# Kernel tuning notes

Hardware: AMD Instinct MI355X
Metric: run time of the kernel (lower is better)

Reference implementation:

```python
import jax, jax.numpy as jnp
import numpy as np

D_MODEL = 1024
N_HEADS = 16
D_K = D_MODEL // N_HEADS

def setup_inputs() -> dict:
    key = jax.random.key(0)
    ks = jax.random.split(key, 9)
    s = 1.0 / np.sqrt(D_MODEL)
    inp = {"x": jax.random.normal(ks[0], (2, 2048, D_MODEL), dtype=jnp.float32)}
    for i, name in enumerate(["q", "k", "v", "o"]):
        inp[f"W{name}"] = jax.random.uniform(ks[1 + i], (D_MODEL, D_MODEL), dtype=jnp.float32, minval=-s, maxval=s)
        inp[f"b{name}"] = jax.random.uniform(ks[5 + i], (D_MODEL,), dtype=jnp.float32, minval=-s, maxval=s)
    return inp

def _split_heads(t):
    B, S, _ = t.shape
    return t.reshape(B, S, N_HEADS, D_K).transpose(0, 2, 1, 3)  # [B,H,S,d_k]

def reference(x, Wq, bq, Wk, bk, Wv, bv, Wo, bo):
    # QKV projections (torch Linear: x @ W.T + b)
    q = _split_heads(x @ Wq.T + bq)
    k = _split_heads(x @ Wk.T + bk)
    v = _split_heads(x @ Wv.T + bv)
    scores = jnp.einsum('bhqd,bhkd->bhqk', q, k) / jnp.sqrt(jnp.asarray(D_K, x.dtype))
    probs = jax.nn.softmax(scores, axis=-1)
    attn = jnp.einsum('bhqk,bhkd->bhqd', probs, v)  # [B,H,S,d_k]
    B, H, S, _ = attn.shape
    merged = attn.transpose(0, 2, 1, 3).reshape(B, S, D_MODEL)
    return merged @ Wo.T + bo
```

## Files before the change

kernel.cpp:

```cpp
#include <hip/hip_runtime.h>
#include <hip/hip_bf16.h>
#include <stdint.h>


#define LOG2E 1.4426950408889634f

typedef float f32x4 __attribute__((ext_vector_type(4)));
typedef float f32x16 __attribute__((ext_vector_type(16)));
typedef short bf16x8 __attribute__((ext_vector_type(8)));
typedef short bf16x4 __attribute__((ext_vector_type(4)));
typedef unsigned int u32x2 __attribute__((ext_vector_type(2)));

__device__ __forceinline__ unsigned short f2bf(float f) {
  __hip_bfloat16 h = __float2bfloat16(f);
  return reinterpret_cast<unsigned short&>(h);
}

#define GLDS(g, l) __builtin_amdgcn_global_load_lds(                          \
    (const __attribute__((address_space(1))) void*)(g),                       \
    (__attribute__((address_space(3))) void*)(l), 16, 0, 0)

__global__ __launch_bounds__(256) void k_conv(const float* __restrict__ src,
                                              unsigned short* __restrict__ dst,
                                              int n4, float scale) {
  int i = blockIdx.x * 256 + threadIdx.x;
  const int stride = gridDim.x * 256;
  for (; i < n4; i += stride) {
    float4 v = ((const float4*)src)[i];
    ushort4 o;
    o.x = f2bf(v.x * scale);
    o.y = f2bf(v.y * scale);
    o.z = f2bf(v.z * scale);
    o.w = f2bf(v.w * scale);
    ((ushort4*)dst)[i] = o;
  }
}

__global__ __launch_bounds__(256) void k_convW(const float* __restrict__ wq,
                                               const float* __restrict__ wk,
                                               const float* __restrict__ wv,
                                               const float* __restrict__ wo,
                                               unsigned short* __restrict__ dq,
                                               unsigned short* __restrict__ dk,
                                               unsigned short* __restrict__ dv,
                                               unsigned short* __restrict__ dw) {
  const int m = blockIdx.y;
  const float* src = (m == 0) ? wq : (m == 1) ? wk : (m == 2) ? wv : wo;
  unsigned short* dst = (m == 0) ? dq : (m == 1) ? dk : (m == 2) ? dv : dw;
  const float scale = (m == 0) ? (0.125f * LOG2E) : 1.0f;
  int i = blockIdx.x * 256 + threadIdx.x;
  float4 v = ((const float4*)src)[i];
  ushort4 o;
  o.x = f2bf(v.x * scale);
  o.y = f2bf(v.y * scale);
  o.z = f2bf(v.z * scale);
  o.w = f2bf(v.w * scale);
  ((ushort4*)dst)[i] = o;
}

__global__ __launch_bounds__(256) void k_bias(const float* __restrict__ bq,
                                              const float* __restrict__ bk,
                                              const float* __restrict__ bv,
                                              float* __restrict__ out) {
  int i = blockIdx.x * 256 + threadIdx.x;
  float v;
  if (i < 1024) v = bq[i] * (0.125f * LOG2E);
  else if (i < 2048) v = bk[i - 1024];
  else v = bv[i - 2048];
  out[i] = v;
}

template <int MODE>
__global__ __launch_bounds__(256) void k_gemm(const unsigned short* __restrict__ A,
                                              const unsigned short* __restrict__ B,
                                              const float* __restrict__ bias,
                                              void* __restrict__ outp) {
  __shared__ unsigned short As[128 * 32];
  __shared__ unsigned short Bs[128 * 32];
  const int tid = threadIdx.x;
  const int lane = tid & 63, wid = tid >> 6;
  const int wr = wid >> 1, wc = wid & 1;
  const int r = lane & 15, g = lane >> 4;
  const int bm = blockIdx.x, bn = blockIdx.y;

  const unsigned short* gA = A + (size_t)bm * 128 * 1024;
  const unsigned short* gB = B + (size_t)bn * 128 * 1024;
  const int row0 = tid >> 2, cg = (tid & 3) * 8;

  f32x4 acc[4][4] = {};

  for (int k0 = 0; k0 < 1024; k0 += 32) {
    __syncthreads();
    GLDS(gA + (size_t)row0 * 1024 + k0 + cg,        As + row0 * 32 + cg);
    GLDS(gA + (size_t)(row0 + 64) * 1024 + k0 + cg, As + (row0 + 64) * 32 + cg);
    GLDS(gB + (size_t)row0 * 1024 + k0 + cg,        Bs + row0 * 32 + cg);
    GLDS(gB + (size_t)(row0 + 64) * 1024 + k0 + cg, Bs + (row0 + 64) * 32 + cg);
    __syncthreads();

    bf16x8 af[4], bfr[4];
#pragma unroll
    for (int i = 0; i < 4; i++) {
      af[i]  = *(const bf16x8*)(As + (wr * 64 + i * 16 + r) * 32 + g * 8);
      bfr[i] = *(const bf16x8*)(Bs + (wc * 64 + i * 16 + r) * 32 + g * 8);
    }
#pragma unroll
    for (int i = 0; i < 4; i++)
#pragma unroll
      for (int j = 0; j < 4; j++)
        acc[i][j] = __builtin_amdgcn_mfma_f32_16x16x32_bf16(af[i], bfr[j], acc[i][j], 0, 0, 0);
  }

#pragma unroll
  for (int i = 0; i < 4; i++) {
    const int rowb = bm * 128 + wr * 64 + i * 16 + g * 4;
#pragma unroll
    for (int j = 0; j < 4; j++) {
      const int col = bn * 128 + wc * 64 + j * 16 + r;
      const float bv = bias[col];
#pragma unroll
      for (int t = 0; t < 4; t++) {
        const int row = rowb + t;
        const float val = acc[i][j][t] + bv;
        if (MODE == 0) {
          const int mat = col >> 10, nn = col & 1023;
          const int hh = nn >> 6, dd = nn & 63;
          const int bb = row >> 11, ss = row & 2047;
          size_t idx;
          if (mat == 2)
            idx = (size_t)2 * 4194304 + (size_t)((bb * 16 + hh) * 64 + dd) * 2048 + ss;
          else
            idx = (size_t)mat * 4194304 + (size_t)((bb * 16 + hh) * 2048 + ss) * 64 + dd;
          ((unsigned short*)outp)[idx] = f2bf(val);
        } else {
          ((float*)outp)[(size_t)row * 1024 + col] = val;
        }
      }
    }
  }
}

__global__ __launch_bounds__(512, 4) void k_attn(const unsigned short* __restrict__ Q,
                                                 const unsigned short* __restrict__ Km,
                                                 const unsigned short* __restrict__ Vt,
                                                 unsigned short* __restrict__ merged) {
  __shared__ unsigned short Kb[2][2][4096];
  __shared__ unsigned short Vb[2][2][4096];
  const int tid = threadIdx.x;
  const int kg = tid >> 8, gtid = tid & 255;
  const int lane = tid & 63, w = (tid >> 6) & 3;
  const int l31 = lane & 31, hi = lane >> 5;
  const int bh = blockIdx.y;
  const int b = bh >> 4, h = bh & 15;
  const int q0 = blockIdx.x * 128;

  const unsigned short* Qh  = Q  + (size_t)bh * 131072;
  const unsigned short* KhG = Km + (size_t)bh * 131072 + (size_t)kg * 65536;
  const unsigned short* VtG = Vt + (size_t)bh * 131072 + 1024 * kg;

  const int qrow = q0 + w * 32 + l31;
  bf16x8 bQ[4];
#pragma unroll
  for (int c = 0; c < 4; c++)
    bQ[c] = *(const bf16x8*)(Qh + (size_t)qrow * 64 + c * 16 + hi * 8);

  int ksrc[2], vsrc[2];
#pragma unroll
  for (int op = 0; op < 2; op++) {
    const int ck = op * 256 + gtid;
    const int s = ck >> 8, c = (ck >> 6) & 3, l2 = ck & 63;
    ksrc[op] = (s * 32 + (l2 & 31)) * 64 + c * 16 + (l2 >> 5) * 8;
    vsrc[op] = (s * 32 + (l2 & 31)) * 2048 + c * 16 + (l2 >> 5) * 8;
  }
  const int ldst = gtid * 8;

  GLDS(KhG + ksrc[0], &Kb[kg][0][ldst]);
  GLDS(KhG + ksrc[1], &Kb[kg][0][2048 + ldst]);
  GLDS(VtG + vsrc[0], &Vb[kg][0][ldst]);
  GLDS(VtG + vsrc[1], &Vb[kg][0][2048 + ldst]);
  __syncthreads();

  f32x16 o0 = {0.f,0.f,0.f,0.f,0.f,0.f,0.f,0.f,0.f,0.f,0.f,0.f,0.f,0.f,0.f,0.f};
  f32x16 o1 = o0;
  float lsum = 0.f;

  for (int t = 0; t < 16; ++t) {
    const int cur = t & 1;
    if (t < 15) {
      const size_t kv = (size_t)(t + 1) * 64;
      GLDS(KhG + kv * 64 + ksrc[0], &Kb[kg][cur ^ 1][ldst]);
      GLDS(KhG + kv * 64 + ksrc[1], &Kb[kg][cur ^ 1][2048 + ldst]);
      GLDS(VtG + kv + vsrc[0], &Vb[kg][cur ^ 1][ldst]);
      GLDS(VtG + kv + vsrc[1], &Vb[kg][cur ^ 1][2048 + ldst]);
    }

    const unsigned short* kb = &Kb[kg][cur][0];
    const unsigned short* vb = &Vb[kg][cur][0];

#define SUBTILE(SC)                                                            \
    {                                                                          \
      bf16x8 kf0 = *(const bf16x8*)(kb + (((SC)*4 + 0) * 64 + lane) * 8);      \
      bf16x8 kf1 = *(const bf16x8*)(kb + (((SC)*4 + 1) * 64 + lane) * 8);      \
      bf16x8 kf2 = *(const bf16x8*)(kb + (((SC)*4 + 2) * 64 + lane) * 8);      \
      bf16x8 kf3 = *(const bf16x8*)(kb + (((SC)*4 + 3) * 64 + lane) * 8);      \
      f32x16 St = {0.f,0.f,0.f,0.f,0.f,0.f,0.f,0.f,                            \
                   0.f,0.f,0.f,0.f,0.f,0.f,0.f,0.f};                           \
      St = __builtin_amdgcn_mfma_f32_32x32x16_bf16(kf0, bQ[0], St, 0, 0, 0);   \
      St = __builtin_amdgcn_mfma_f32_32x32x16_bf16(kf1, bQ[1], St, 0, 0, 0);   \
      St = __builtin_amdgcn_mfma_f32_32x32x16_bf16(kf2, bQ[2], St, 0, 0, 0);   \
      St = __builtin_amdgcn_mfma_f32_32x32x16_bf16(kf3, bQ[3], St, 0, 0, 0);   \
      float p[16];                                                             \
      float ps = 0.f;                                                          \
      _Pragma("unroll")                                                        \
      for (int u = 0; u < 16; u++) {                                           \
        p[u] = __builtin_amdgcn_exp2f(St[u]);                                  \
        ps += p[u];                                                            \
      }                                                                        \
      lsum += ps;                                                              \
      unsigned int a0, a1, b0, b1;                                             \
      asm("v_cvt_pk_bf16_f32 %0, %1, %2" : "=v"(a0) : "v"(p[0]), "v"(p[1]));   \
      asm("v_cvt_pk_bf16_f32 %0, %1, %2" : "=v"(a1) : "v"(p[2]), "v"(p[3]));   \
      asm("v_cvt_pk_bf16_f32 %0, %1, %2" : "=v"(b0) : "v"(p[4]), "v"(p[5]));   \
      asm("v_cvt_pk_bf16_f32 %0, %1, %2" : "=v"(b1) : "v"(p[6]), "v"(p[7]));   \
      u32x2 r0 = __builtin_amdgcn_permlane32_swap(a0, b0, false, false);       \
      u32x2 r1 = __builtin_amdgcn_permlane32_swap(a1, b1, false, false);       \
      union { unsigned int u[4]; bf16x8 v; } pfE;                              \
      pfE.u[0] = r0[0]; pfE.u[1] = r1[0]; pfE.u[2] = r0[1]; pfE.u[3] = r1[1];  \
      asm("v_cvt_pk_bf16_f32 %0, %1, %2" : "=v"(a0) : "v"(p[8]), "v"(p[9]));   \
      asm("v_cvt_pk_bf16_f32 %0, %1, %2" : "=v"(a1) : "v"(p[10]), "v"(p[11])); \
      asm("v_cvt_pk_bf16_f32 %0, %1, %2" : "=v"(b0) : "v"(p[12]), "v"(p[13])); \
      asm("v_cvt_pk_bf16_f32 %0, %1, %2" : "=v"(b1) : "v"(p[14]), "v"(p[15])); \
      r0 = __builtin_amdgcn_permlane32_swap(a0, b0, false, false);             \
      r1 = __builtin_amdgcn_permlane32_swap(a1, b1, false, false);             \
      union { unsigned int u[4]; bf16x8 v; } pfO;                              \
      pfO.u[0] = r0[0]; pfO.u[1] = r1[0]; pfO.u[2] = r0[1]; pfO.u[3] = r1[1];  \
      bf16x8 v00 = *(const bf16x8*)(vb + ((0 + 2*(SC)) * 64 + lane) * 8);      \
      bf16x8 v01 = *(const bf16x8*)(vb + ((1 + 2*(SC)) * 64 + lane) * 8);      \
      bf16x8 v10 = *(const bf16x8*)(vb + ((4 + 2*(SC)) * 64 + lane) * 8);      \
      bf16x8 v11 = *(const bf16x8*)(vb + ((5 + 2*(SC)) * 64 + lane) * 8);      \
      o0 = __builtin_amdgcn_mfma_f32_32x32x16_bf16(v00, pfE.v, o0, 0, 0, 0);   \
      o0 = __builtin_amdgcn_mfma_f32_32x32x16_bf16(v01, pfO.v, o0, 0, 0, 0);   \
      o1 = __builtin_amdgcn_mfma_f32_32x32x16_bf16(v10, pfE.v, o1, 0, 0, 0);   \
      o1 = __builtin_amdgcn_mfma_f32_32x32x16_bf16(v11, pfO.v, o1, 0, 0, 0);   \
    }

    SUBTILE(0)
    SUBTILE(1)
#undef SUBTILE

    __syncthreads();
  }

  float* lbuf = (float*)&Vb[0][0][0];
  char*  ob   = (char*)&Kb[0][0][0] + gtid * 128;
  const unsigned sw2 = ((unsigned)(gtid & 7)) << 4;
  if (kg == 1) {
#pragma unroll
    for (int j = 0; j < 4; j++) {
      float4 t0 = { o0[4*j], o0[4*j+1], o0[4*j+2], o0[4*j+3] };
      *(float4*)(ob + (((unsigned)(j * 16)) ^ sw2)) = t0;
    }
#pragma unroll
    for (int j = 0; j < 4; j++) {
      float4 t1 = { o1[4*j], o1[4*j+1], o1[4*j+2], o1[4*j+3] };
      *(float4*)(ob + (((unsigned)(64 + j * 16)) ^ sw2)) = t1;
    }
    lbuf[gtid] = lsum;
  }
  __syncthreads();
  if (kg == 0) {
#pragma unroll
    for (int j = 0; j < 4; j++) {
      float4 t0 = *(const float4*)(ob + (((unsigned)(j * 16)) ^ sw2));
      o0[4*j] += t0.x; o0[4*j+1] += t0.y; o0[4*j+2] += t0.z; o0[4*j+3] += t0.w;
    }
#pragma unroll
    for (int j = 0; j < 4; j++) {
      float4 t1 = *(const float4*)(ob + (((unsigned)(64 + j * 16)) ^ sw2));
      o1[4*j] += t1.x; o1[4*j+1] += t1.y; o1[4*j+2] += t1.z; o1[4*j+3] += t1.w;
    }
    lsum += lbuf[gtid];

    const float inv = 1.0f / (lsum + __shfl_xor(lsum, 32));
    const size_t base = (size_t)(b * 2048 + qrow) * 1024 + h * 64;
#pragma unroll
    for (int ds = 0; ds < 2; ds++) {
      const f32x16& oo = ds ? o1 : o0;
#pragma unroll
      for (int m = 0; m < 4; m++) {
        bf16x4 ov;
#pragma unroll
        for (int i = 0; i < 4; i++) ov[i] = (short)f2bf(oo[m * 4 + i] * inv);
        *(bf16x4*)(&merged[base + ds * 32 + m * 8 + hi * 4]) = ov;
      }
    }
  }
}

extern "C" void kernel_launch(void* const* d_in, const int* in_sizes, int n_in,
                              void* d_out, int out_size, void* d_ws, size_t ws_size,
                              hipStream_t stream) {
  const float* x  = (const float*)d_in[0];
  const float* Wq = (const float*)d_in[1];
  const float* bq = (const float*)d_in[2];
  const float* Wk = (const float*)d_in[3];
  const float* bk = (const float*)d_in[4];
  const float* Wv = (const float*)d_in[5];
  const float* bv = (const float*)d_in[6];
  const float* Wo = (const float*)d_in[7];
  const float* bo = (const float*)d_in[8];

  if (ws_size < (size_t)50343936) return;

  unsigned short* ws  = (unsigned short*)d_ws;
  unsigned short* xb  = ws;
  unsigned short* Wb  = ws + 4194304;
  unsigned short* Wob = ws + 7340032;
  unsigned short* qkv = ws + 8388608;
  unsigned short* mrg = ws + 20971520;
  float* biasQ = (float*)(ws + 25165824);

  k_conv<<<dim3(2048), dim3(256), 0, stream>>>(x, xb, 1048576, 1.0f);
  k_convW<<<dim3(1024, 4), dim3(256), 0, stream>>>(Wq, Wk, Wv, Wo,
      Wb, Wb + 1048576, Wb + 2097152, Wob);
  k_bias<<<dim3(12), dim3(256), 0, stream>>>(bq, bk, bv, biasQ);

  k_gemm<0><<<dim3(32, 24), dim3(256), 0, stream>>>(xb, Wb, biasQ, (void*)qkv);
  k_attn<<<dim3(16, 32), dim3(512), 0, stream>>>(qkv, qkv + 4194304, qkv + 8388608, mrg);
  k_gemm<1><<<dim3(32, 8), dim3(256), 0, stream>>>(mrg, Wob, bo, d_out);
}
```

Before: 136.2 us.

## Split attention KV halves into separate blocks, merge via atomics, defer normalization

Each 512-thread attention block, which reduced two KV halves through shared memory, becomes two independent 256-thread blocks along grid z. Each block atomically adds its unnormalized fp32 output and row sum into global buffers, which are cleared with memsets first. The output-projection GEMM now reads the fp32 merged tensor, divides by the row sum and converts to bf16 while staging A tiles. The aim is more, smaller blocks and no in-block reduction, at the cost of fp32 atomic traffic, extra memsets and a heavier, unpipelined A load in the final GEMM.

```diff
diff --git a/kernel.cpp b/kernel.cpp
--- a/kernel.cpp
+++ b/kernel.cpp
@@ -70,11 +70,10 @@
   out[i] = v;
 }
 
-template <int MODE>
-__global__ __launch_bounds__(256) void k_gemm(const unsigned short* __restrict__ A,
-                                              const unsigned short* __restrict__ B,
-                                              const float* __restrict__ bias,
-                                              void* __restrict__ outp) {
+__global__ __launch_bounds__(256) void k_gemm0(const unsigned short* __restrict__ A,
+                                               const unsigned short* __restrict__ B,
+                                               const float* __restrict__ bias,
+                                               unsigned short* __restrict__ outp) {
   __shared__ unsigned short As[128 * 32];
   __shared__ unsigned short Bs[128 * 32];
   const int tid = threadIdx.x;
@@ -121,37 +120,106 @@
       for (int t = 0; t < 4; t++) {
         const int row = rowb + t;
         const float val = acc[i][j][t] + bv;
-        if (MODE == 0) {
-          const int mat = col >> 10, nn = col & 1023;
-          const int hh = nn >> 6, dd = nn & 63;
-          const int bb = row >> 11, ss = row & 2047;
-          size_t idx;
-          if (mat == 2)
-            idx = (size_t)2 * 4194304 + (size_t)((bb * 16 + hh) * 64 + dd) * 2048 + ss;
-          else
-            idx = (size_t)mat * 4194304 + (size_t)((bb * 16 + hh) * 2048 + ss) * 64 + dd;
-          ((unsigned short*)outp)[idx] = f2bf(val);
-        } else {
-          ((float*)outp)[(size_t)row * 1024 + col] = val;
-        }
+        const int mat = col >> 10, nn = col & 1023;
+        const int hh = nn >> 6, dd = nn & 63;
+        const int bb = row >> 11, ss = row & 2047;
+        size_t idx;
+        if (mat == 2)
+          idx = (size_t)2 * 4194304 + (size_t)((bb * 16 + hh) * 64 + dd) * 2048 + ss;
+        else
+          idx = (size_t)mat * 4194304 + (size_t)((bb * 16 + hh) * 2048 + ss) * 64 + dd;
+        outp[idx] = f2bf(val);
       }
     }
   }
 }
 
-__global__ __launch_bounds__(512, 4) void k_attn(const unsigned short* __restrict__ Q,
-                                                 const unsigned short* __restrict__ Km,
-                                                 const unsigned short* __restrict__ Vt,
-                                                 unsigned short* __restrict__ merged) {
-  __shared__ unsigned short Kb[2][2][4096];
-  __shared__ unsigned short Vb[2][2][4096];
+__global__ __launch_bounds__(256) void k_gemm1(const float* __restrict__ A,
+                                               const float* __restrict__ lG,
+                                               const unsigned short* __restrict__ Bw,
+                                               const float* __restrict__ bias,
+                                               float* __restrict__ outp) {
+  __shared__ unsigned short As[128 * 32];
+  __shared__ unsigned short Bs[128 * 32];
   const int tid = threadIdx.x;
-  const int kg = tid >> 8, gtid = tid & 255;
-  const int lane = tid & 63, w = (tid >> 6) & 3;
+  const int lane = tid & 63, wid = tid >> 6;
+  const int wr = wid >> 1, wc = wid & 1;
+  const int r = lane & 15, g = lane >> 4;
+  const int bm = blockIdx.x, bn = blockIdx.y;
+
+  const unsigned short* gB = Bw + (size_t)bn * 128 * 1024;
+  const int row0 = tid >> 2, cg = (tid & 3) * 8;
+  const int gr0 = bm * 128 + row0, gr1 = gr0 + 64;
+  const int s0g = gr0 & 2047, b0g = gr0 >> 11;
+  const int s1g = gr1 & 2047, b1g = gr1 >> 11;
+
+  f32x4 acc[4][4] = {};
+
+  for (int k0 = 0; k0 < 1024; k0 += 32) {
+    const int hh = (k0 + cg) >> 6;
+    const float li0 = 1.0f / lG[(b0g * 16 + hh) * 2048 + s0g];
+    const float li1 = 1.0f / lG[(b1g * 16 + hh) * 2048 + s1g];
+    const float4 a00 = *(const float4*)(A + (size_t)gr0 * 1024 + k0 + cg);
+    const float4 a01 = *(const float4*)(A + (size_t)gr0 * 1024 + k0 + cg + 4);
+    const float4 a10 = *(const float4*)(A + (size_t)gr1 * 1024 + k0 + cg);
+    const float4 a11 = *(const float4*)(A + (size_t)gr1 * 1024 + k0 + cg + 4);
+    __syncthreads();
+    GLDS(gB + (size_t)row0 * 1024 + k0 + cg,        Bs + row0 * 32 + cg);
+    GLDS(gB + (size_t)(row0 + 64) * 1024 + k0 + cg, Bs + (row0 + 64) * 32 + cg);
+    bf16x8 pa0, pa1;
+    pa0[0] = f2bf(a00.x * li0); pa0[1] = f2bf(a00.y * li0);
+    pa0[2] = f2bf(a00.z * li0); pa0[3] = f2bf(a00.w * li0);
+    pa0[4] = f2bf(a01.x * li0); pa0[5] = f2bf(a01.y * li0);
+    pa0[6] = f2bf(a01.z * li0); pa0[7] = f2bf(a01.w * li0);
+    pa1[0] = f2bf(a10.x * li1); pa1[1] = f2bf(a10.y * li1);
+    pa1[2] = f2bf(a10.z * li1); pa1[3] = f2bf(a10.w * li1);
+    pa1[4] = f2bf(a11.x * li1); pa1[5] = f2bf(a11.y * li1);
+    pa1[6] = f2bf(a11.z * li1); pa1[7] = f2bf(a11.w * li1);
+    *(bf16x8*)(As + row0 * 32 + cg) = pa0;
+    *(bf16x8*)(As + (row0 + 64) * 32 + cg) = pa1;
+    __syncthreads();
+
+    bf16x8 af[4], bfr[4];
+#pragma unroll
+    for (int i = 0; i < 4; i++) {
+      af[i]  = *(const bf16x8*)(As + (wr * 64 + i * 16 + r) * 32 + g * 8);
+      bfr[i] = *(const bf16x8*)(Bs + (wc * 64 + i * 16 + r) * 32 + g * 8);
+    }
+#pragma unroll
+    for (int i = 0; i < 4; i++)
+#pragma unroll
+      for (int j = 0; j < 4; j++)
+        acc[i][j] = __builtin_amdgcn_mfma_f32_16x16x32_bf16(af[i], bfr[j], acc[i][j], 0, 0, 0);
+  }
+
+#pragma unroll
+  for (int i = 0; i < 4; i++) {
+    const int rowb = bm * 128 + wr * 64 + i * 16 + g * 4;
+#pragma unroll
+    for (int j = 0; j < 4; j++) {
+      const int col = bn * 128 + wc * 64 + j * 16 + r;
+      const float bv = bias[col];
+#pragma unroll
+      for (int t = 0; t < 4; t++)
+        outp[(size_t)(rowb + t) * 1024 + col] = acc[i][j][t] + bv;
+    }
+  }
+}
+
+__global__ __launch_bounds__(256) void k_attn(const unsigned short* __restrict__ Q,
+                                              const unsigned short* __restrict__ Km,
+                                              const unsigned short* __restrict__ Vt,
+                                              float* __restrict__ mrgF,
+                                              float* __restrict__ lG) {
+  __shared__ unsigned short Kb[2][4096];
+  __shared__ unsigned short Vb[2][4096];
+  const int tid = threadIdx.x;
+  const int lane = tid & 63, w = tid >> 6;
   const int l31 = lane & 31, hi = lane >> 5;
   const int bh = blockIdx.y;
   const int b = bh >> 4, h = bh & 15;
   const int q0 = blockIdx.x * 128;
+  const int kg = blockIdx.z;
 
   const unsigned short* Qh  = Q  + (size_t)bh * 131072;
   const unsigned short* KhG = Km + (size_t)bh * 131072 + (size_t)kg * 65536;
@@ -166,17 +234,17 @@
   int ksrc[2], vsrc[2];
 #pragma unroll
   for (int op = 0; op < 2; op++) {
-    const int ck = op * 256 + gtid;
+    const int ck = op * 256 + tid;
     const int s = ck >> 8, c = (ck >> 6) & 3, l2 = ck & 63;
     ksrc[op] = (s * 32 + (l2 & 31)) * 64 + c * 16 + (l2 >> 5) * 8;
     vsrc[op] = (s * 32 + (l2 & 31)) * 2048 + c * 16 + (l2 >> 5) * 8;
   }
-  const int ldst = gtid * 8;
-
-  GLDS(KhG + ksrc[0], &Kb[kg][0][ldst]);
-  GLDS(KhG + ksrc[1], &Kb[kg][0][2048 + ldst]);
-  GLDS(VtG + vsrc[0], &Vb[kg][0][ldst]);
-  GLDS(VtG + vsrc[1], &Vb[kg][0][2048 + ldst]);
+  const int ldst = tid * 8;
+
+  GLDS(KhG + ksrc[0], &Kb[0][ldst]);
+  GLDS(KhG + ksrc[1], &Kb[0][2048 + ldst]);
+  GLDS(VtG + vsrc[0], &Vb[0][ldst]);
+  GLDS(VtG + vsrc[1], &Vb[0][2048 + ldst]);
   __syncthreads();
 
   f32x16 o0 = {0.f,0.f,0.f,0.f,0.f,0.f,0.f,0.f,0.f,0.f,0.f,0.f,0.f,0.f,0.f,0.f};
@@ -187,14 +255,14 @@
     const int cur = t & 1;
     if (t < 15) {
       const size_t kv = (size_t)(t + 1) * 64;
-      GLDS(KhG + kv * 64 + ksrc[0], &Kb[kg][cur ^ 1][ldst]);
-      GLDS(KhG + kv * 64 + ksrc[1], &Kb[kg][cur ^ 1][2048 + ldst]);
-      GLDS(VtG + kv + vsrc[0], &Vb[kg][cur ^ 1][ldst]);
-      GLDS(VtG + kv + vsrc[1], &Vb[kg][cur ^ 1][2048 + ldst]);
-    }
-
-    const unsigned short* kb = &Kb[kg][cur][0];
-    const unsigned short* vb = &Vb[kg][cur][0];
+      GLDS(KhG + kv * 64 + ksrc[0], &Kb[cur ^ 1][ldst]);
+      GLDS(KhG + kv * 64 + ksrc[1], &Kb[cur ^ 1][2048 + ldst]);
+      GLDS(VtG + kv + vsrc[0], &Vb[cur ^ 1][ldst]);
+      GLDS(VtG + kv + vsrc[1], &Vb[cur ^ 1][2048 + ldst]);
+    }
+
+    const unsigned short* kb = &Kb[cur][0];
+    const unsigned short* vb = &Vb[cur][0];
 
 #define SUBTILE(SC)                                                            \
     {                                                                          \
@@ -250,49 +318,17 @@
     __syncthreads();
   }
 
-  float* lbuf = (float*)&Vb[0][0][0];
-  char*  ob   = (char*)&Kb[0][0][0] + gtid * 128;
-  const unsigned sw2 = ((unsigned)(gtid & 7)) << 4;
-  if (kg == 1) {
-#pragma unroll
-    for (int j = 0; j < 4; j++) {
-      float4 t0 = { o0[4*j], o0[4*j+1], o0[4*j+2], o0[4*j+3] };
-      *(float4*)(ob + (((unsigned)(j * 16)) ^ sw2)) = t0;
-    }
-#pragma unroll
-    for (int j = 0; j < 4; j++) {
-      float4 t1 = { o1[4*j], o1[4*j+1], o1[4*j+2], o1[4*j+3] };
-      *(float4*)(ob + (((unsigned)(64 + j * 16)) ^ sw2)) = t1;
-    }
-    lbuf[gtid] = lsum;
-  }
-  __syncthreads();
-  if (kg == 0) {
-#pragma unroll
-    for (int j = 0; j < 4; j++) {
-      float4 t0 = *(const float4*)(ob + (((unsigned)(j * 16)) ^ sw2));
-      o0[4*j] += t0.x; o0[4*j+1] += t0.y; o0[4*j+2] += t0.z; o0[4*j+3] += t0.w;
-    }
-#pragma unroll
-    for (int j = 0; j < 4; j++) {
-      float4 t1 = *(const float4*)(ob + (((unsigned)(64 + j * 16)) ^ sw2));
-      o1[4*j] += t1.x; o1[4*j+1] += t1.y; o1[4*j+2] += t1.z; o1[4*j+3] += t1.w;
-    }
-    lsum += lbuf[gtid];
-
-    const float inv = 1.0f / (lsum + __shfl_xor(lsum, 32));
-    const size_t base = (size_t)(b * 2048 + qrow) * 1024 + h * 64;
-#pragma unroll
-    for (int ds = 0; ds < 2; ds++) {
-      const f32x16& oo = ds ? o1 : o0;
-#pragma unroll
-      for (int m = 0; m < 4; m++) {
-        bf16x4 ov;
-#pragma unroll
-        for (int i = 0; i < 4; i++) ov[i] = (short)f2bf(oo[m * 4 + i] * inv);
-        *(bf16x4*)(&merged[base + ds * 32 + m * 8 + hi * 4]) = ov;
-      }
-    }
+  const float lrow = lsum + __shfl_xor(lsum, 32);
+  if (hi == 0) atomicAdd(&lG[bh * 2048 + qrow], lrow);
+  const size_t base = (size_t)(b * 2048 + qrow) * 1024 + h * 64;
+#pragma unroll
+  for (int ds = 0; ds < 2; ds++) {
+    const f32x16& oo = ds ? o1 : o0;
+#pragma unroll
+    for (int m = 0; m < 4; m++)
+#pragma unroll
+      for (int i = 0; i < 4; i++)
+        atomicAdd(&mrgF[base + ds * 32 + m * 8 + hi * 4 + i], oo[m * 4 + i]);
   }
 }
 
@@ -309,22 +345,28 @@
   const float* Wo = (const float*)d_in[7];
   const float* bo = (const float*)d_in[8];
 
-  if (ws_size < (size_t)50343936) return;
+  if (ws_size < (size_t)44314624) return;
 
   unsigned short* ws  = (unsigned short*)d_ws;
   unsigned short* xb  = ws;
   unsigned short* Wb  = ws + 4194304;
-  unsigned short* Wob = ws + 7340032;
   unsigned short* qkv = ws + 8388608;
-  unsigned short* mrg = ws + 20971520;
-  float* biasQ = (float*)(ws + 25165824);
+  unsigned short* Wob = ws + 20971520;
+  float* biasQ = (float*)(ws + 22020096);
+  float* lG    = (float*)(ws + 22026240);
+  float* mrgF  = (float*)ws;
 
   k_conv<<<dim3(2048), dim3(256), 0, stream>>>(x, xb, 1048576, 1.0f);
   k_convW<<<dim3(1024, 4), dim3(256), 0, stream>>>(Wq, Wk, Wv, Wo,
       Wb, Wb + 1048576, Wb + 2097152, Wob);
   k_bias<<<dim3(12), dim3(256), 0, stream>>>(bq, bk, bv, biasQ);
 
-  k_gemm<0><<<dim3(32, 24), dim3(256), 0, stream>>>(xb, Wb, biasQ, (void*)qkv);
-  k_attn<<<dim3(16, 32), dim3(512), 0, stream>>>(qkv, qkv + 4194304, qkv + 8388608, mrg);
-  k_gemm<1><<<dim3(32, 8), dim3(256), 0, stream>>>(mrg, Wob, bo, d_out);
-}
+  k_gemm0<<<dim3(32, 24), dim3(256), 0, stream>>>(xb, Wb, biasQ, qkv);
+
+  hipMemsetAsync(mrgF, 0, (size_t)4194304 * 4, stream);
+  hipMemsetAsync(lG, 0, (size_t)65536 * 4, stream);
+
+  k_attn<<<dim3(16, 32, 2), dim3(256), 0, stream>>>(
+      qkv, qkv + 4194304, qkv + 8388608, mrgF, lG);
+  k_gemm1<<<dim3(32, 8), dim3(256), 0, stream>>>(mrgF, lG, Wob, bo, (float*)d_out);
+}
```

Result: slower. 339.7 us (+149.4%).
